# Kernel optimization log

Measured on AMD Instinct MI355X. Metric: run time of the kernel, lower is better.

The kernel has to match this reference:

```python
import jax, jax.numpy as jnp
import numpy as np
import math

B, S, D = 32, 512, 1024
H = 16
DH = D // H
L = 4
DFF = 2048
DMEM = 512
EPS = 1e-5


def _pos_encoding(seq_len, d_model):
    # sinusoidal PE, shape [seq_len, 1, d_model]
    position = jnp.arange(seq_len, dtype=jnp.float32)[:, None]
    div_term = jnp.exp(jnp.arange(0, d_model, 2, dtype=jnp.float32) * (-math.log(10000.0) / d_model))
    pe = jnp.zeros((seq_len, d_model), dtype=jnp.float32)
    pe = pe.at[:, 0::2].set(jnp.sin(position * div_term))
    pe = pe.at[:, 1::2].set(jnp.cos(position * div_term))
    return pe[:, None, :]


def _layer_norm(x, g, b):
    mu = jnp.mean(x, axis=-1, keepdims=True)
    var = jnp.mean(jnp.square(x - mu), axis=-1, keepdims=True)
    return (x - mu) * jax.lax.rsqrt(var + EPS) * g + b


def setup_inputs() -> dict:
    key = jax.random.key(0)
    ks = jax.random.split(key, 8)
    w = 0.02  # weight scale for stable deep stack
    return {
        "x": jax.random.normal(ks[0], (B, S, D), dtype=jnp.float32),
        "Wqkv": jax.random.normal(ks[1], (L, 3 * D, D), dtype=jnp.float32) * w,
        "bqkv": jnp.zeros((L, 3 * D), dtype=jnp.float32),
        "Wo": jax.random.normal(ks[2], (L, D, D), dtype=jnp.float32) * w,
        "bo": jnp.zeros((L, D), dtype=jnp.float32),
        "W1": jax.random.normal(ks[3], (L, DFF, D), dtype=jnp.float32) * w,
        "b1": jnp.zeros((L, DFF), dtype=jnp.float32),
        "W2": jax.random.normal(ks[4], (L, D, DFF), dtype=jnp.float32) * w,
        "b2": jnp.zeros((L, D), dtype=jnp.float32),
        "ln1_g": jnp.ones((L, D), dtype=jnp.float32),
        "ln1_b": jnp.zeros((L, D), dtype=jnp.float32),
        "ln2_g": jnp.ones((L, D), dtype=jnp.float32),
        "ln2_b": jnp.zeros((L, D), dtype=jnp.float32),
        "normf_g": jnp.ones((D,), dtype=jnp.float32),
        "normf_b": jnp.zeros((D,), dtype=jnp.float32),
        "Wout": jax.random.normal(ks[5], (DMEM, D), dtype=jnp.float32) * w,
        "bout": jnp.zeros((DMEM,), dtype=jnp.float32),
    }


def reference(x, Wqkv, bqkv, Wo, bo, W1, b1, W2, b2,
              ln1_g, ln1_b, ln2_g, ln2_b, normf_g, normf_b, Wout, bout):
    # x: [B, S, D] -> [S, B, D]
    h = jnp.transpose(x, (1, 0, 2))
    h = h + _pos_encoding(S, D)  # dropout p=0 in eval
    scale = 1.0 / math.sqrt(DH)
    for l in range(L):
        # --- self-attention block (post-norm) ---
        qkv = h @ Wqkv[l].T + bqkv[l]          # [S, B, 3D]
        q, k, v = jnp.split(qkv, 3, axis=-1)
        q = q.reshape(S, B, H, DH)
        k = k.reshape(S, B, H, DH)
        v = v.reshape(S, B, H, DH)
        scores = jnp.einsum('sbhd,tbhd->bhst', q, k) * scale  # [B, H, S, S]
        attn = jax.nn.softmax(scores, axis=-1)
        ctx = jnp.einsum('bhst,tbhd->sbhd', attn, v).reshape(S, B, D)
        sa = ctx @ Wo[l].T + bo[l]
        h = _layer_norm(h + sa, ln1_g[l], ln1_b[l])
        # --- feed-forward block (post-norm) ---
        ff = jax.nn.relu(h @ W1[l].T + b1[l]) @ W2[l].T + b2[l]
        h = _layer_norm(h + ff, ln2_g[l], ln2_b[l])
    h = _layer_norm(h, normf_g, normf_b)       # encoder final norm
    h = jnp.transpose(h, (1, 0, 2))            # [B, S, D]
    return h @ Wout.T + bout                   # [B, S, DMEM]
```

## Files before the change

### kernel.cpp

```cpp
#include <hip/hip_runtime.h>

#define BB    32
#define SS    512
#define DD    1024
#define HH_   16
#define DH    64
#define LL    4
#define DFF   2048
#define DMEM  512
#define NTOK  (BB * SS)
#define SPLD  74

typedef __attribute__((ext_vector_type(8))) short short8;
typedef __attribute__((ext_vector_type(4))) float f32x4;

__device__ __forceinline__ unsigned short f2bf(float x) {
    unsigned u = __float_as_uint(x);
    u = (u + 0x7FFFu + ((u >> 16) & 1u)) >> 16;
    return (unsigned short)u;
}
__device__ __forceinline__ float bf2f(unsigned short x) {
    return __uint_as_float(((unsigned)x) << 16);
}

__device__ __forceinline__ void async16(const unsigned short* g, unsigned short* l) {
    __builtin_amdgcn_global_load_lds(
        (__attribute__((address_space(1))) void*)g,
        (__attribute__((address_space(3))) void*)l,
        16, 0, 0);
}

__global__ void cvt_bf16(const float* __restrict__ in, unsigned short* __restrict__ out, int n) {
    int i4 = (blockIdx.x * 256 + threadIdx.x) * 4;
    if (i4 < n) {
        float4 v = *(const float4*)&in[i4];
        uint2 pk;
        pk.x = f2bf(v.x) | ((unsigned)f2bf(v.y) << 16);
        pk.y = f2bf(v.z) | ((unsigned)f2bf(v.w) << 16);
        *(uint2*)&out[i4] = pk;
    }
}

__global__ void add_pe_kernel(const float* __restrict__ x,
                              unsigned short* __restrict__ hb) {
    int i4 = (blockIdx.x * 256 + threadIdx.x) * 4;
    int d = i4 & (DD - 1);
    int t = i4 >> 10;
    int s = t & (SS - 1);
    const float c = -9.210340371976184f / (float)DD;
    float f0 = __expf((float)d * c);
    float f2 = __expf((float)(d + 2) * c);
    float a0 = (float)s * f0, a2 = (float)s * f2;
    float4 xv = *(const float4*)&x[i4];
    uint2 pk;
    pk.x = f2bf(xv.x + __sinf(a0)) | ((unsigned)f2bf(xv.y + __cosf(a0)) << 16);
    pk.y = f2bf(xv.z + __sinf(a2)) | ((unsigned)f2bf(xv.w + __cosf(a2)) << 16);
    *(uint2*)&hb[i4] = pk;
}

#define BAR   __builtin_amdgcn_s_barrier()
#define LGKM0 do { asm volatile("s_waitcnt lgkmcnt(0)" ::: "memory"); \
                   __builtin_amdgcn_sched_barrier(0); } while (0)
#define VMC4  asm volatile("s_waitcnt vmcnt(4)" ::: "memory")

#define STAGE(BUF, OP, HALFI, KS) do {                                          \
    const unsigned short* _g = (OP) ? Wb : A;                                   \
    const size_t _gr = ((OP) ? Brow0 : Arow0) + (HALFI) * 128 + wid * 16 + l8;  \
    unsigned short* _d = &lds[BUF][OP][(((HALFI) * 128 + wid * 16)) * 64];      \
    const int _ks = (KS);                                                       \
    async16(&_g[_gr * (size_t)K + _ks + cl8], _d);                              \
    async16(&_g[(_gr + 8) * (size_t)K + _ks + cl8], _d + 8 * 64);               \
} while (0)

#define HALF_ITER(CUR, OTH, KS1, KS2) {                                         \
    short8 afr[4][2], b01[2][2], b23[2][2];                                     \
    _Pragma("unroll") for (int m = 0; m < 4; m++) {                             \
        afr[m][0] = *(const short8*)&lds[CUR][0][aro + m * 1024 + cb0];         \
        afr[m][1] = *(const short8*)&lds[CUR][0][aro + m * 1024 + cb1]; }       \
    _Pragma("unroll") for (int n = 0; n < 2; n++) {                             \
        b01[n][0] = *(const short8*)&lds[CUR][1][bro + n * 1024 + cb0];         \
        b01[n][1] = *(const short8*)&lds[CUR][1][bro + n * 1024 + cb1]; }       \
    STAGE(OTH, 0, 0, KS1);                                                      \
    BAR; LGKM0;                                                                 \
    __builtin_amdgcn_s_setprio(1);                                              \
    _Pragma("unroll") for (int m = 0; m < 4; m++)                               \
        _Pragma("unroll") for (int n = 0; n < 2; n++) {                         \
            acc[m][n] = __builtin_amdgcn_mfma_f32_16x16x32_bf16(b01[n][0], afr[m][0], acc[m][n], 0, 0, 0); \
            acc[m][n] = __builtin_amdgcn_mfma_f32_16x16x32_bf16(b01[n][1], afr[m][1], acc[m][n], 0, 0, 0); } \
    __builtin_amdgcn_s_setprio(0);                                              \
    BAR;                                                                        \
    _Pragma("unroll") for (int n = 0; n < 2; n++) {                             \
        b23[n][0] = *(const short8*)&lds[CUR][1][bro + (n + 2) * 1024 + cb0];   \
        b23[n][1] = *(const short8*)&lds[CUR][1][bro + (n + 2) * 1024 + cb1]; } \
    STAGE(OTH, 0, 1, KS1);                                                      \
    BAR; LGKM0;                                                                 \
    __builtin_amdgcn_s_setprio(1);                                              \
    _Pragma("unroll") for (int m = 0; m < 4; m++)                               \
        _Pragma("unroll") for (int n = 0; n < 2; n++) {                         \
            acc[m][n + 2] = __builtin_amdgcn_mfma_f32_16x16x32_bf16(b23[n][0], afr[m][0], acc[m][n + 2], 0, 0, 0); \
            acc[m][n + 2] = __builtin_amdgcn_mfma_f32_16x16x32_bf16(b23[n][1], afr[m][1], acc[m][n + 2], 0, 0, 0); } \
    __builtin_amdgcn_s_setprio(0);                                              \
    BAR;                                                                        \
    _Pragma("unroll") for (int m = 0; m < 4; m++) {                             \
        afr[m][0] = *(const short8*)&lds[CUR][0][aro + (m + 4) * 1024 + cb0];   \
        afr[m][1] = *(const short8*)&lds[CUR][0][aro + (m + 4) * 1024 + cb1]; } \
    STAGE(CUR, 1, 0, KS2);                                                      \
    BAR; LGKM0;                                                                 \
    __builtin_amdgcn_s_setprio(1);                                              \
    _Pragma("unroll") for (int m = 0; m < 4; m++)                               \
        _Pragma("unroll") for (int n = 0; n < 2; n++) {                         \
            acc[m + 4][n + 2] = __builtin_amdgcn_mfma_f32_16x16x32_bf16(b23[n][0], afr[m][0], acc[m + 4][n + 2], 0, 0, 0); \
            acc[m + 4][n + 2] = __builtin_amdgcn_mfma_f32_16x16x32_bf16(b23[n][1], afr[m][1], acc[m + 4][n + 2], 0, 0, 0); } \
    __builtin_amdgcn_s_setprio(0);                                              \
    BAR;                                                                        \
    STAGE(CUR, 1, 1, KS2);                                                      \
    VMC4;                                                                       \
    BAR;                                                                        \
    __builtin_amdgcn_s_setprio(1);                                              \
    _Pragma("unroll") for (int m = 0; m < 4; m++)                               \
        _Pragma("unroll") for (int n = 0; n < 2; n++) {                         \
            acc[m + 4][n] = __builtin_amdgcn_mfma_f32_16x16x32_bf16(b01[n][0], afr[m][0], acc[m + 4][n], 0, 0, 0); \
            acc[m + 4][n] = __builtin_amdgcn_mfma_f32_16x16x32_bf16(b01[n][1], afr[m][1], acc[m + 4][n], 0, 0, 0); } \
    __builtin_amdgcn_s_setprio(0);                                              \
    BAR;                                                                        \
}

template<bool RELU>
__global__ __launch_bounds__(512, 2) void gemm_bt8(
    const unsigned short* __restrict__ A,
    const unsigned short* __restrict__ Wb,
    const float* __restrict__ bias,
    float* __restrict__ Cf, unsigned short* __restrict__ Cb,
    int M, int N, int K)
{
    __shared__ __align__(16) unsigned short lds[2][2][256 * 64];
    const int tid  = threadIdx.x;
    const int wid  = tid >> 6, lane = tid & 63;
    const int wm   = wid >> 2, wn = wid & 3;
    const int quad = lane >> 4, l16 = lane & 15;
    const int l8   = lane >> 3;
    const int cl8  = (((lane & 7) ^ l8) & 7) * 8;
    const int bm   = blockIdx.y, bn = blockIdx.x;
    const size_t Arow0 = (size_t)bm * 256, Brow0 = (size_t)bn * 256;

    const int swz = l16 & 7;
    const int cb0 = ((quad) ^ swz) * 8;
    const int cb1 = ((4 + quad) ^ swz) * 8;
    const int aro = (wm * 128 + l16) * 64;
    const int bro = (wn * 64 + l16) * 64;

    f32x4 acc[8][4];
    #pragma unroll
    for (int i = 0; i < 8; i++)
        #pragma unroll
        for (int j = 0; j < 4; j++) acc[i][j] = (f32x4){0.f, 0.f, 0.f, 0.f};

    STAGE(0, 1, 0, 0);  STAGE(0, 1, 1, 0);
    STAGE(0, 0, 0, 0);  STAGE(0, 0, 1, 0);
    STAGE(1, 1, 0, 64); STAGE(1, 1, 1, 64);
    VMC4;
    BAR;

    for (int k0 = 0; k0 < K; k0 += 128) {
        const int ksb = (k0 + 128 < K) ? (k0 + 128) : (K - 64);
        const int ksc = (k0 + 192 < K) ? (k0 + 192) : (K - 64);
        HALF_ITER(0, 1, k0 + 64, ksb)
        HALF_ITER(1, 0, ksb, ksc)
    }

    #pragma unroll
    for (int i = 0; i < 8; i++) {
        const size_t mrow = (size_t)(bm * 256 + wm * 128 + i * 16 + l16) * N;
        #pragma unroll
        for (int j = 0; j < 4; j++) {
            int n0 = bn * 256 + wn * 64 + j * 16 + quad * 4;
            f32x4 av = acc[i][j];
            float v[4];
            if (bias) {
                float4 bv = *(const float4*)&bias[n0];
                v[0] = av[0] + bv.x; v[1] = av[1] + bv.y;
                v[2] = av[2] + bv.z; v[3] = av[3] + bv.w;
            } else {
                v[0] = av[0]; v[1] = av[1]; v[2] = av[2]; v[3] = av[3];
            }
            if (RELU) {
                #pragma unroll
                for (int r = 0; r < 4; r++) v[r] = fmaxf(v[r], 0.f);
            }
            if (Cf) {
                float4 o4; o4.x = v[0]; o4.y = v[1]; o4.z = v[2]; o4.w = v[3];
                *(float4*)&Cf[mrow + n0] = o4;
            }
            if (Cb) {
                uint2 pk;
                pk.x = f2bf(v[0]) | ((unsigned)f2bf(v[1]) << 16);
                pk.y = f2bf(v[2]) | ((unsigned)f2bf(v[3]) << 16);
                *(uint2*)&Cb[mrow + n0] = pk;
            }
        }
    }
}

template<bool RELU, bool WPRE>
__global__ __launch_bounds__(256) void gemm_bt(
    const unsigned short* __restrict__ A,
    const unsigned short* __restrict__ Wb,
    const float* __restrict__ Wf,
    const float* __restrict__ bias,
    float* __restrict__ Cf, unsigned short* __restrict__ Cb,
    int M, int N, int K)
{
    __shared__ __align__(16) unsigned short As[128 * 32];
    __shared__ __align__(16) unsigned short Bs[128 * 32];
    const int tid  = threadIdx.x;
    const int bm   = blockIdx.y, bn = blockIdx.x;
    const int w    = tid >> 6, lane = tid & 63;
    const int wm   = (w >> 1) * 64, wn = (w & 1) * 64;
    const int quad = lane >> 4, l16 = lane & 15;

    f32x4 acc[4][4];
    #pragma unroll
    for (int i = 0; i < 4; i++)
        #pragma unroll
        for (int j = 0; j < 4; j++) acc[i][j] = (f32x4){0.f, 0.f, 0.f, 0.f};

    const int rlane = lane >> 2, clane = (lane & 3) * 8;

    for (int k0 = 0; k0 < K; k0 += 32) {
        __syncthreads();
        if (WPRE) {
            #pragma unroll
            for (int i = 0; i < 2; i++) {
                int j = w * 2 + i;
                async16(&A [(size_t)(bm * 128 + j * 16 + rlane) * K + k0 + clane], &As[j * 512]);
                async16(&Wb[(size_t)(bn * 128 + j * 16 + rlane) * K + k0 + clane], &Bs[j * 512]);
            }
        } else {
            #pragma unroll
            for (int u = 0; u < 2; u++) {
                int c = tid * 2 + u;
                int row = c >> 2, cc = (c & 3) * 8;
                *(uint4*)&As[row * 32 + cc] =
                    *(const uint4*)&A[(size_t)(bm * 128 + row) * K + k0 + cc];
                const float* wp = &Wf[(size_t)(bn * 128 + row) * K + k0 + cc];
                float4 w0 = *(const float4*)wp;
                float4 w1 = *(const float4*)(wp + 4);
                uint4 pk;
                pk.x = ((unsigned)f2bf(w0.y) << 16) | f2bf(w0.x);
                pk.y = ((unsigned)f2bf(w0.w) << 16) | f2bf(w0.z);
                pk.z = ((unsigned)f2bf(w1.y) << 16) | f2bf(w1.x);
                pk.w = ((unsigned)f2bf(w1.w) << 16) | f2bf(w1.z);
                *(uint4*)&Bs[row * 32 + cc] = pk;
            }
        }
        __syncthreads();
        short8 af[4], bfr[4];
        #pragma unroll
        for (int i = 0; i < 4; i++)
            af[i] = *(const short8*)&As[(wm + i * 16 + l16) * 32 + quad * 8];
        #pragma unroll
        for (int j = 0; j < 4; j++)
            bfr[j] = *(const short8*)&Bs[(wn + j * 16 + l16) * 32 + quad * 8];
        #pragma unroll
        for (int i = 0; i < 4; i++)
            #pragma unroll
            for (int j = 0; j < 4; j++)
                acc[i][j] = __builtin_amdgcn_mfma_f32_16x16x32_bf16(bfr[j], af[i], acc[i][j], 0, 0, 0);
    }

    #pragma unroll
    for (int i = 0; i < 4; i++) {
        const size_t mrow = (size_t)(bm * 128 + wm + i * 16 + l16) * N;
        #pragma unroll
        for (int j = 0; j < 4; j++) {
            int n0 = bn * 128 + wn + j * 16 + quad * 4;
            f32x4 av = acc[i][j];
            float v[4];
            if (bias) {
                float4 bv = *(const float4*)&bias[n0];
                v[0] = av[0] + bv.x; v[1] = av[1] + bv.y;
                v[2] = av[2] + bv.z; v[3] = av[3] + bv.w;
            } else {
                v[0] = av[0]; v[1] = av[1]; v[2] = av[2]; v[3] = av[3];
            }
            if (RELU) {
                #pragma unroll
                for (int r = 0; r < 4; r++) v[r] = fmaxf(v[r], 0.f);
            }
            if (Cf) {
                float4 o4; o4.x = v[0]; o4.y = v[1]; o4.z = v[2]; o4.w = v[3];
                *(float4*)&Cf[mrow + n0] = o4;
            }
            if (Cb) {
                uint2 pk;
                pk.x = f2bf(v[0]) | ((unsigned)f2bf(v[1]) << 16);
                pk.y = f2bf(v[2]) | ((unsigned)f2bf(v[3]) << 16);
                *(uint2*)&Cb[mrow + n0] = pk;
            }
        }
    }
}

__global__ __launch_bounds__(256) void attn_kernel(const unsigned short* __restrict__ qkv,
                                                   unsigned short* __restrict__ ctx)
{
    __shared__ __align__(16) unsigned short sK [64 * SPLD];
    __shared__ __align__(16) unsigned short sVt[64 * SPLD];
    __shared__ __align__(16) unsigned short sP [128 * SPLD];

    const int tid  = threadIdx.x;
    const int blk  = blockIdx.x;
    const int qt   = blk & 3;
    const int hh   = (blk >> 2) & 15;
    const int b    = blk >> 6;
    const int w    = tid >> 6, lane = tid & 63;
    const int quad = lane >> 4, l16 = lane & 15;
    const size_t rowbase = (size_t)b * SS;
    const int LDQ = 3 * DD;

    short8 qf[2][2];
    #pragma unroll
    for (int m = 0; m < 2; m++) {
        const unsigned short* qrow =
            qkv + (rowbase + qt * 128 + w * 32 + m * 16 + l16) * (size_t)LDQ + hh * 64;
        #pragma unroll
        for (int kk = 0; kk < 2; kk++) {
            uint4 q4 = *(const uint4*)&qrow[kk * 32 + quad * 8];
            unsigned short* qs = (unsigned short*)&q4;
            short8 f;
            short* fp = (short*)&f;
            #pragma unroll
            for (int e = 0; e < 8; e++) fp[e] = (short)f2bf(bf2f(qs[e]) * 0.125f);
            qf[m][kk] = f;
        }
    }

    float l_part[2] = {0.f, 0.f};
    f32x4 o[2][4];
    #pragma unroll
    for (int m = 0; m < 2; m++)
        #pragma unroll
        for (int nt = 0; nt < 4; nt++) o[m][nt] = (f32x4){0.f, 0.f, 0.f, 0.f};

    for (int kt = 0; kt < 8; kt++) {
        __syncthreads();
        #pragma unroll
        for (int u = 0; u < 2; u++) {
            int c = tid * 2 + u;
            int r = c >> 3, cc = (c & 7) * 8;
            const size_t src = (rowbase + kt * 64 + r) * (size_t)LDQ + hh * 64 + cc;
            *(uint4*)&sK[r * SPLD + cc] = *(const uint4*)&qkv[src + DD];
            uint4 v4 = *(const uint4*)&qkv[src + 2 * DD];
            unsigned short* vs = (unsigned short*)&v4;
            #pragma unroll
            for (int e = 0; e < 8; e++) sVt[(cc + e) * SPLD + r] = vs[e];
        }
        __syncthreads();

        #pragma unroll
        for (int m = 0; m < 2; m++) {
            f32x4 s[4];
            #pragma unroll
            for (int ct = 0; ct < 4; ct++) s[ct] = (f32x4){0.f, 0.f, 0.f, 0.f};
            #pragma unroll
            for (int kk = 0; kk < 2; kk++)
                #pragma unroll
                for (int ct = 0; ct < 4; ct++) {
                    short8 kb = *(const short8*)&sK[(ct * 16 + l16) * SPLD + kk * 32 + quad * 8];
                    s[ct] = __builtin_amdgcn_mfma_f32_16x16x32_bf16(kb, qf[m][kk], s[ct], 0, 0, 0);
                }
            const int prow = (w * 32 + m * 16 + l16) * SPLD;
            float lp = 0.f;
            #pragma unroll
            for (int ct = 0; ct < 4; ct++) {
                float p0 = __expf(fminf(s[ct][0], 30.f));
                float p1 = __expf(fminf(s[ct][1], 30.f));
                float p2 = __expf(fminf(s[ct][2], 30.f));
                float p3 = __expf(fminf(s[ct][3], 30.f));
                lp += (p0 + p1) + (p2 + p3);
                uint2 pk;
                pk.x = f2bf(p0) | ((unsigned)f2bf(p1) << 16);
                pk.y = f2bf(p2) | ((unsigned)f2bf(p3) << 16);
                *(uint2*)&sP[prow + ct * 16 + quad * 4] = pk;
            }
            l_part[m] += lp;
        }

        #pragma unroll
        for (int m = 0; m < 2; m++)
            #pragma unroll
            for (int kk = 0; kk < 2; kk++) {
                short8 pa = *(const short8*)&sP[(w * 32 + m * 16 + l16) * SPLD + kk * 32 + quad * 8];
                #pragma unroll
                for (int nt = 0; nt < 4; nt++) {
                    short8 vb = *(const short8*)&sVt[(nt * 16 + l16) * SPLD + kk * 32 + quad * 8];
                    o[m][nt] = __builtin_amdgcn_mfma_f32_16x16x32_bf16(vb, pa, o[m][nt], 0, 0, 0);
                }
            }
    }

    #pragma unroll
    for (int m = 0; m < 2; m++) {
        float lt = l_part[m];
        lt += __shfl_xor(lt, 16);
        lt += __shfl_xor(lt, 32);
        float inv = 1.f / lt;
        const size_t crow = (rowbase + qt * 128 + w * 32 + m * 16 + l16) * DD + hh * 64;
        #pragma unroll
        for (int nt = 0; nt < 4; nt++) {
            uint2 pk;
            pk.x = f2bf(o[m][nt][0] * inv) | ((unsigned)f2bf(o[m][nt][1] * inv) << 16);
            pk.y = f2bf(o[m][nt][2] * inv) | ((unsigned)f2bf(o[m][nt][3] * inv) << 16);
            *(uint2*)&ctx[crow + nt * 16 + quad * 4] = pk;
        }
    }
}

__global__ __launch_bounds__(256) void ln_kernel(
    unsigned short* __restrict__ hb, const unsigned short* __restrict__ add,
    const float* __restrict__ g, const float* __restrict__ beta)
{
    __shared__ float sred[4];
    const int t = blockIdx.x, tid = threadIdx.x;
    const int d0 = tid * 4;
    const size_t base = (size_t)t * DD + d0;
    float x[4];
    {
        uint2 hv = *(const uint2*)&hb[base];
        x[0] = bf2f(hv.x & 0xFFFF); x[1] = bf2f(hv.x >> 16);
        x[2] = bf2f(hv.y & 0xFFFF); x[3] = bf2f(hv.y >> 16);
    }
    if (add) {
        uint2 av = *(const uint2*)&add[base];
        x[0] += bf2f(av.x & 0xFFFF); x[1] += bf2f(av.x >> 16);
        x[2] += bf2f(av.y & 0xFFFF); x[3] += bf2f(av.y >> 16);
    }
    float s = (x[0] + x[1]) + (x[2] + x[3]);
    #pragma unroll
    for (int off = 32; off > 0; off >>= 1) s += __shfl_down(s, off);
    if ((tid & 63) == 0) sred[tid >> 6] = s;
    __syncthreads();
    float mu = (sred[0] + sred[1] + sred[2] + sred[3]) * (1.f / DD);
    __syncthreads();
    float vs = 0.f;
    #pragma unroll
    for (int i = 0; i < 4; i++) { float dx = x[i] - mu; vs += dx * dx; }
    #pragma unroll
    for (int off = 32; off > 0; off >>= 1) vs += __shfl_down(vs, off);
    if ((tid & 63) == 0) sred[tid >> 6] = vs;
    __syncthreads();
    float var = (sred[0] + sred[1] + sred[2] + sred[3]) * (1.f / DD);
    float inv = rsqrtf(var + 1e-5f);
    float4 gv = *(const float4*)&g[d0];
    float4 bv = *(const float4*)&beta[d0];
    float y0 = (x[0] - mu) * inv * gv.x + bv.x;
    float y1 = (x[1] - mu) * inv * gv.y + bv.y;
    float y2 = (x[2] - mu) * inv * gv.z + bv.z;
    float y3 = (x[3] - mu) * inv * gv.w + bv.w;
    uint2 pk;
    pk.x = f2bf(y0) | ((unsigned)f2bf(y1) << 16);
    pk.y = f2bf(y2) | ((unsigned)f2bf(y3) << 16);
    *(uint2*)&hb[base] = pk;
}

static void launch_gemm(bool relu, bool pre, const unsigned short* A,
                        const unsigned short* Wb, const float* Wf, const float* bias,
                        float* Cf, unsigned short* Cb, int M, int N, int K, hipStream_t s)
{
    if (pre && (M % 256 == 0) && (N % 256 == 0) && (K % 128 == 0) && N >= 1024) {
        dim3 g8(N / 256, M / 256);
        if (relu) gemm_bt8<true ><<<g8, 512, 0, s>>>(A, Wb, bias, Cf, Cb, M, N, K);
        else      gemm_bt8<false><<<g8, 512, 0, s>>>(A, Wb, bias, Cf, Cb, M, N, K);
        return;
    }
    dim3 g(N / 128, M / 128);
    if (pre) {
        if (relu) gemm_bt<true,  true ><<<g, 256, 0, s>>>(A, Wb, nullptr, bias, Cf, Cb, M, N, K);
        else      gemm_bt<false, true ><<<g, 256, 0, s>>>(A, Wb, nullptr, bias, Cf, Cb, M, N, K);
    } else {
        if (relu) gemm_bt<true,  false><<<g, 256, 0, s>>>(A, nullptr, Wf, bias, Cf, Cb, M, N, K);
        else      gemm_bt<false, false><<<g, 256, 0, s>>>(A, nullptr, Wf, bias, Cf, Cb, M, N, K);
    }
}

extern "C" void kernel_launch(void* const* d_in, const int* in_sizes, int n_in,
                              void* d_out, int out_size, void* d_ws, size_t ws_size,
                              hipStream_t stream)
{
    const float* x    = (const float*)d_in[0];
    const float* Wqkv = (const float*)d_in[1];
    const float* bqkv = (const float*)d_in[2];
    const float* Wo   = (const float*)d_in[3];
    const float* bo   = (const float*)d_in[4];
    const float* W1   = (const float*)d_in[5];
    const float* b1   = (const float*)d_in[6];
    const float* W2   = (const float*)d_in[7];
    const float* b2   = (const float*)d_in[8];
    const float* ln1g = (const float*)d_in[9];
    const float* ln1b = (const float*)d_in[10];
    const float* ln2g = (const float*)d_in[11];
    const float* ln2b = (const float*)d_in[12];
    const float* nfg  = (const float*)d_in[13];
    const float* nfb  = (const float*)d_in[14];
    const float* Wout = (const float*)d_in[15];
    const float* bout = (const float*)d_in[16];
    float* out = (float*)d_out;

    char* ws = (char*)d_ws;
    const size_t MB = 1024 * 1024;
    unsigned short* hb    = (unsigned short*)(ws + 0 * MB);
    unsigned short* qkvb  = (unsigned short*)(ws + 32 * MB);
    unsigned short* tmpb  = (unsigned short*)(ws + 96 * MB);
    unsigned short* ctxb  = (unsigned short*)(ws + 128 * MB);
    unsigned short* WqkvB = (unsigned short*)(ws + 160 * MB);
    unsigned short* W1B   = (unsigned short*)(ws + 184 * MB);
    unsigned short* W2B   = (unsigned short*)(ws + 200 * MB);
    unsigned short* WoB   = (unsigned short*)(ws + 216 * MB);
    unsigned short* WoutB = (unsigned short*)(ws + 224 * MB);

    const bool pre = ws_size >= 225 * MB;
    if (pre) {
        cvt_bf16<<<(LL * 3 * DD * DD / 4 + 255) / 256, 256, 0, stream>>>(Wqkv, WqkvB, LL * 3 * DD * DD);
        cvt_bf16<<<(LL * DFF * DD / 4 + 255) / 256, 256, 0, stream>>>(W1, W1B, LL * DFF * DD);
        cvt_bf16<<<(LL * DD * DFF / 4 + 255) / 256, 256, 0, stream>>>(W2, W2B, LL * DD * DFF);
        cvt_bf16<<<(LL * DD * DD / 4 + 255) / 256, 256, 0, stream>>>(Wo, WoB, LL * DD * DD);
        cvt_bf16<<<(DMEM * DD / 4 + 255) / 256, 256, 0, stream>>>(Wout, WoutB, DMEM * DD);
    }

    add_pe_kernel<<<NTOK * DD / 1024, 256, 0, stream>>>(x, hb);

    for (int l = 0; l < LL; l++) {
        launch_gemm(false, pre, hb, WqkvB + (size_t)l * 3 * DD * DD,
                    Wqkv + (size_t)l * 3 * DD * DD, bqkv + l * 3 * DD,
                    nullptr, qkvb, NTOK, 3 * DD, DD, stream);
        attn_kernel<<<BB * HH_ * 4, 256, 0, stream>>>(qkvb, ctxb);
        launch_gemm(false, pre, ctxb, WoB + (size_t)l * DD * DD,
                    Wo + (size_t)l * DD * DD, bo + l * DD,
                    nullptr, tmpb, NTOK, DD, DD, stream);
        ln_kernel<<<NTOK, 256, 0, stream>>>(hb, tmpb, ln1g + l * DD, ln1b + l * DD);
        launch_gemm(true, pre, hb, W1B + (size_t)l * DFF * DD,
                    W1 + (size_t)l * DFF * DD, b1 + l * DFF,
                    nullptr, qkvb, NTOK, DFF, DD, stream);
        launch_gemm(false, pre, qkvb, W2B + (size_t)l * DD * DFF,
                    W2 + (size_t)l * DD * DFF, b2 + l * DD,
                    nullptr, tmpb, NTOK, DD, DFF, stream);
        ln_kernel<<<NTOK, 256, 0, stream>>>(hb, tmpb, ln2g + l * DD, ln2b + l * DD);
    }
    ln_kernel<<<NTOK, 256, 0, stream>>>(hb, nullptr, nfg, nfb);
    launch_gemm(false, pre, hb, WoutB, Wout, bout, out, nullptr, NTOK, DMEM, DD, stream);
}
```

Before: 2.112 ms.

## Restructure GEMM double-buffer prefetch to full-tile lookahead and add XCD-aware block remap

```diff
diff --git a/kernel.cpp b/kernel.cpp
--- a/kernel.cpp
+++ b/kernel.cpp
@@ -61,7 +61,7 @@
 #define BAR   __builtin_amdgcn_s_barrier()
 #define LGKM0 do { asm volatile("s_waitcnt lgkmcnt(0)" ::: "memory"); \
                    __builtin_amdgcn_sched_barrier(0); } while (0)
-#define VMC4  asm volatile("s_waitcnt vmcnt(4)" ::: "memory")
+#define VMC8  asm volatile("s_waitcnt vmcnt(8)" ::: "memory")
 
 #define STAGE(BUF, OP, HALFI, KS) do {                                          \
     const unsigned short* _g = (OP) ? Wb : A;                                   \
@@ -72,7 +72,7 @@
     async16(&_g[(_gr + 8) * (size_t)K + _ks + cl8], _d + 8 * 64);               \
 } while (0)
 
-#define HALF_ITER(CUR, OTH, KS1, KS2) {                                         \
+#define HALF_ITER(CUR, KSR) {                                                   \
     short8 afr[4][2], b01[2][2], b23[2][2];                                     \
     _Pragma("unroll") for (int m = 0; m < 4; m++) {                             \
         afr[m][0] = *(const short8*)&lds[CUR][0][aro + m * 1024 + cb0];         \
@@ -80,7 +80,6 @@
     _Pragma("unroll") for (int n = 0; n < 2; n++) {                             \
         b01[n][0] = *(const short8*)&lds[CUR][1][bro + n * 1024 + cb0];         \
         b01[n][1] = *(const short8*)&lds[CUR][1][bro + n * 1024 + cb1]; }       \
-    STAGE(OTH, 0, 0, KS1);                                                      \
     BAR; LGKM0;                                                                 \
     __builtin_amdgcn_s_setprio(1);                                              \
     _Pragma("unroll") for (int m = 0; m < 4; m++)                               \
@@ -92,7 +91,6 @@
     _Pragma("unroll") for (int n = 0; n < 2; n++) {                             \
         b23[n][0] = *(const short8*)&lds[CUR][1][bro + (n + 2) * 1024 + cb0];   \
         b23[n][1] = *(const short8*)&lds[CUR][1][bro + (n + 2) * 1024 + cb1]; } \
-    STAGE(OTH, 0, 1, KS1);                                                      \
     BAR; LGKM0;                                                                 \
     __builtin_amdgcn_s_setprio(1);                                              \
     _Pragma("unroll") for (int m = 0; m < 4; m++)                               \
@@ -104,7 +102,8 @@
     _Pragma("unroll") for (int m = 0; m < 4; m++) {                             \
         afr[m][0] = *(const short8*)&lds[CUR][0][aro + (m + 4) * 1024 + cb0];   \
         afr[m][1] = *(const short8*)&lds[CUR][0][aro + (m + 4) * 1024 + cb1]; } \
-    STAGE(CUR, 1, 0, KS2);                                                      \
+    STAGE(CUR, 1, 0, KSR);                                                      \
+    STAGE(CUR, 1, 1, KSR);                                                      \
     BAR; LGKM0;                                                                 \
     __builtin_amdgcn_s_setprio(1);                                              \
     _Pragma("unroll") for (int m = 0; m < 4; m++)                               \
@@ -113,8 +112,9 @@
             acc[m + 4][n + 2] = __builtin_amdgcn_mfma_f32_16x16x32_bf16(b23[n][1], afr[m][1], acc[m + 4][n + 2], 0, 0, 0); } \
     __builtin_amdgcn_s_setprio(0);                                              \
     BAR;                                                                        \
-    STAGE(CUR, 1, 1, KS2);                                                      \
-    VMC4;                                                                       \
+    STAGE(CUR, 0, 0, KSR);                                                      \
+    STAGE(CUR, 0, 1, KSR);                                                      \
+    VMC8;                                                                       \
     BAR;                                                                        \
     __builtin_amdgcn_s_setprio(1);                                              \
     _Pragma("unroll") for (int m = 0; m < 4; m++)                               \
@@ -140,7 +140,12 @@
     const int quad = lane >> 4, l16 = lane & 15;
     const int l8   = lane >> 3;
     const int cl8  = (((lane & 7) ^ l8) & 7) * 8;
-    const int bm   = blockIdx.y, bn = blockIdx.x;
+
+    const int nwgx = gridDim.x;
+    const int nwg  = nwgx * (int)gridDim.y;
+    int orig = blockIdx.y * nwgx + blockIdx.x;
+    int swid = ((nwg & 7) == 0) ? ((orig & 7) * (nwg >> 3) + (orig >> 3)) : orig;
+    const int bm = swid / nwgx, bn = swid % nwgx;
     const size_t Arow0 = (size_t)bm * 256, Brow0 = (size_t)bn * 256;
 
     const int swz = l16 & 7;
@@ -158,14 +163,16 @@
     STAGE(0, 1, 0, 0);  STAGE(0, 1, 1, 0);
     STAGE(0, 0, 0, 0);  STAGE(0, 0, 1, 0);
     STAGE(1, 1, 0, 64); STAGE(1, 1, 1, 64);
-    VMC4;
+    STAGE(1, 0, 0, 64); STAGE(1, 0, 1, 64);
+    VMC8;
     BAR;
 
-    for (int k0 = 0; k0 < K; k0 += 128) {
-        const int ksb = (k0 + 128 < K) ? (k0 + 128) : (K - 64);
-        const int ksc = (k0 + 192 < K) ? (k0 + 192) : (K - 64);
-        HALF_ITER(0, 1, k0 + 64, ksb)
-        HALF_ITER(1, 0, ksb, ksc)
+    const int NT = K >> 6;
+    for (int t = 0; t < NT; t += 2) {
+        const int ks0 = ((t + 2 < NT) ? (t + 2) : (NT - 1)) * 64;
+        const int ks1 = ((t + 3 < NT) ? (t + 3) : (NT - 1)) * 64;
+        HALF_ITER(0, ks0)
+        HALF_ITER(1, ks1)
     }
 
     #pragma unroll
```

Result: faster. 2.025 ms (-4.1%).
